# Optimization experiments

Measured on AMD Instinct MI355X. Metric: run time of the kernel, lower is better.

Reference implementation:

```python
import jax, jax.numpy as jnp
import numpy as np

BS, T, HS, WS = 2, 4, 32, 32
HW = HS * WS
D, NH, NL, NP = 256, 8, 4, 4
HD = D // NH
DFFN = 1024


def layer_norm(x, g, b, eps=1e-5):
    mu = jnp.mean(x, axis=-1, keepdims=True)
    var = jnp.mean((x - mu) ** 2, axis=-1, keepdims=True)
    return (x - mu) * jax.lax.rsqrt(var + eps) * g + b


def bilinear_gather(val, loc, Hl, Wl):
    # val: (bs, nh, Hl*Wl, hd); loc: (bs, Lq, nh, P, 2) in [0,1], last dim (x, y)
    # matches F.grid_sample(align_corners=False, padding_mode='zeros') on grid=2*loc-1
    x = loc[..., 0] * Wl - 0.5
    y = loc[..., 1] * Hl - 0.5
    x0 = jnp.floor(x)
    y0 = jnp.floor(y)
    lx = x - x0
    ly = y - y0
    bs, Lq, nh, P = x.shape
    out = jnp.zeros((bs, nh, Lq * P, val.shape[-1]), val.dtype)
    for dy in (0, 1):
        for dx in (0, 1):
            xi = x0 + dx
            yi = y0 + dy
            w = (lx if dx else 1.0 - lx) * (ly if dy else 1.0 - ly)
            valid = (xi >= 0) & (xi < Wl) & (yi >= 0) & (yi < Hl)
            w = jnp.where(valid, w, 0.0)
            xi_c = jnp.clip(xi, 0, Wl - 1).astype(jnp.int32)
            yi_c = jnp.clip(yi, 0, Hl - 1).astype(jnp.int32)
            idx = (yi_c * Wl + xi_c).transpose(0, 2, 1, 3).reshape(bs, nh, Lq * P)
            g = jnp.take_along_axis(val, idx[..., None], axis=2)
            wt = w.transpose(0, 2, 1, 3).reshape(bs, nh, Lq * P)
            out = out + wt[..., None] * g
    return out.reshape(bs, nh, Lq, P, val.shape[-1])


def setup_inputs() -> dict:
    key = jax.random.key(0)
    ks = jax.random.split(key, 12)
    s = 0.02
    return {
        "src": jax.random.normal(ks[0], (BS, T, HW, D), jnp.float32),
        "pos": jax.random.normal(ks[1], (BS, T, HW, D), jnp.float32),
        "reference_points": jax.random.uniform(ks[2], (BS, T * HW, NL, 2), jnp.float32),
        "value_proj_w": jax.random.normal(ks[3], (D, D), jnp.float32) * s,
        "value_proj_b": jnp.zeros((D,), jnp.float32),
        "sampling_offsets_w": jax.random.normal(ks[4], (D, NH * NL * NP * 2), jnp.float32) * s,
        "sampling_offsets_b": jax.random.normal(ks[5], (NH * NL * NP * 2,), jnp.float32) * s,
        "attn_weights_w": jax.random.normal(ks[6], (D, NH * NL * NP), jnp.float32) * s,
        "attn_weights_b": jnp.zeros((NH * NL * NP,), jnp.float32),
        "output_proj_w": jax.random.normal(ks[7], (D, D), jnp.float32) * s,
        "output_proj_b": jnp.zeros((D,), jnp.float32),
        "norm1_g": jnp.ones((D,), jnp.float32),
        "norm1_b": jnp.zeros((D,), jnp.float32),
        "linear1_w": jax.random.normal(ks[8], (D, DFFN), jnp.float32) * s,
        "linear1_b": jnp.zeros((DFFN,), jnp.float32),
        "linear2_w": jax.random.normal(ks[9], (DFFN, D), jnp.float32) * s,
        "linear2_b": jnp.zeros((D,), jnp.float32),
        "norm2_g": jnp.ones((D,), jnp.float32),
        "norm2_b": jnp.zeros((D,), jnp.float32),
        "spatial_shapes": np.array([[HS, WS]] * NL, np.int32),
        "level_start_index": np.arange(NL, dtype=np.int32) * HW,
    }


def reference(src, pos, reference_points, value_proj_w, value_proj_b,
              sampling_offsets_w, sampling_offsets_b, attn_weights_w, attn_weights_b,
              output_proj_w, output_proj_b, norm1_g, norm1_b,
              linear1_w, linear1_b, linear2_w, linear2_b, norm2_g, norm2_b,
              spatial_shapes, level_start_index):
    bs, t, hw, d = src.shape
    Lq = t * hw
    x = src.reshape(bs, Lq, d)
    q = x  # module never adds pos in forward (with_pos_embed unused)
    value = (x @ value_proj_w + value_proj_b).reshape(bs, Lq, NH, HD)
    offsets = (q @ sampling_offsets_w + sampling_offsets_b).reshape(bs, Lq, NH, NL, NP, 2)
    aw = jax.nn.softmax((q @ attn_weights_w + attn_weights_b).reshape(bs, Lq, NH, NL * NP), axis=-1)
    aw = aw.reshape(bs, Lq, NH, NL, NP)
    ss = np.asarray(spatial_shapes)
    lsi = np.asarray(level_start_index)
    offset_normalizer = jnp.asarray(ss[:, ::-1].copy(), src.dtype)  # (L, 2) = (W, H)
    sampling_locations = reference_points[:, :, None, :, None, :] + offsets / offset_normalizer[None, None, None, :, None, :]
    attn_out = jnp.zeros((bs, NH, Lq, HD), src.dtype)
    for l in range(NL):
        Hl, Wl = int(ss[l, 0]), int(ss[l, 1])
        start = int(lsi[l])
        v_l = value[:, start:start + Hl * Wl].transpose(0, 2, 1, 3)  # (bs, nh, HlWl, hd)
        samp = bilinear_gather(v_l, sampling_locations[:, :, :, l], Hl, Wl)  # (bs, nh, Lq, P, hd)
        w_l = aw[:, :, :, l].transpose(0, 2, 1, 3)  # (bs, nh, Lq, P)
        attn_out = attn_out + jnp.sum(samp * w_l[..., None], axis=3)
    attn_out = attn_out.transpose(0, 2, 1, 3).reshape(bs, Lq, d) @ output_proj_w + output_proj_b
    x = layer_norm(x + attn_out, norm1_g, norm1_b)
    ffn = jax.nn.relu(x @ linear1_w + linear1_b) @ linear2_w + linear2_b
    x = layer_norm(x + ffn, norm2_g, norm2_b)
    return x.reshape(bs, t, hw, d), sampling_locations
```

## Files before the change

### kernel.cpp

```cpp
#include <hip/hip_runtime.h>
#include <math.h>

#define ROWS   8192
#define LQ     4096
#define NHEAD  8
#define NLVL   4
#define NPTS   4
#define HDIM   32

typedef __attribute__((ext_vector_type(8))) short v8s;
typedef __attribute__((ext_vector_type(4))) float v4f;

__device__ __forceinline__ unsigned short f2bf(float x) {
    unsigned int u = __float_as_uint(x);
    u += 0x7fffu + ((u >> 16) & 1u);
    return (unsigned short)(u >> 16);
}
__device__ __forceinline__ float bf2f(unsigned short x) {
    return __uint_as_float(((unsigned int)x) << 16);
}

__device__ __forceinline__ void glds16(const void* g, void* l) {
    __builtin_amdgcn_global_load_lds(
        (const __attribute__((address_space(1))) unsigned int*)g,
        (__attribute__((address_space(3))) unsigned int*)l, 16, 0, 0);
}

__device__ __forceinline__ void trans_tile(const float* __restrict__ in,
                                           unsigned short* __restrict__ out,
                                           int K, int N, int ldout, int n_off,
                                           int bx, int by, int tid)
{
    __shared__ float t[32][33];
    int tx = tid & 31, ty = tid >> 5;
    int k0 = by << 5, n0 = bx << 5;
    #pragma unroll
    for (int i = 0; i < 4; i++)
        t[ty + i * 8][tx] = in[(size_t)(k0 + ty + i * 8) * N + n0 + tx];
    __syncthreads();
    #pragma unroll
    for (int i = 0; i < 4; i++)
        out[(size_t)(n_off + n0 + ty + i * 8) * ldout + k0 + tx] = f2bf(t[tx][ty + i * 8]);
}

__global__ __launch_bounds__(256) void prep_k(
    const float* __restrict__ src, unsigned short* __restrict__ src_bf,
    const float* __restrict__ vw, const float* __restrict__ ofw,
    const float* __restrict__ aww, const float* __restrict__ pw,
    const float* __restrict__ w1, const float* __restrict__ w2,
    unsigned short* __restrict__ Btcat, unsigned short* __restrict__ pwT,
    unsigned short* __restrict__ w1T, unsigned short* __restrict__ w2T,
    const float* __restrict__ vb, const float* __restrict__ ofb,
    const float* __restrict__ awb, float* __restrict__ biascat)
{
    int bid = blockIdx.x, tid = threadIdx.x;
    if (bid < 2048) {
        int i = bid * 256 + tid;
        float4 v = ((const float4*)src)[i];
        ushort4 o;
        o.x = f2bf(v.x); o.y = f2bf(v.y); o.z = f2bf(v.z); o.w = f2bf(v.w);
        ((ushort4*)src_bf)[i] = o;
    } else if (bid < 2112) {
        int t = bid - 2048; trans_tile(vw, Btcat, 256, 256, 256, 0, t & 7, t >> 3, tid);
    } else if (bid < 2176) {
        int t = bid - 2112; trans_tile(ofw, Btcat, 256, 256, 256, 256, t & 7, t >> 3, tid);
    } else if (bid < 2208) {
        int t = bid - 2176; trans_tile(aww, Btcat, 256, 128, 256, 512, t & 3, t >> 2, tid);
    } else if (bid < 2272) {
        int t = bid - 2208; trans_tile(pw, pwT, 256, 256, 256, 0, t & 7, t >> 3, tid);
    } else if (bid < 2528) {
        int t = bid - 2272; trans_tile(w1, w1T, 256, 1024, 256, 0, t & 31, t >> 5, tid);
    } else if (bid < 2784) {
        int t = bid - 2528; trans_tile(w2, w2T, 1024, 256, 1024, 0, t & 7, t >> 3, tid);
    } else {
        biascat[tid] = vb[tid];
        biascat[tid + 256] = ofb[tid];
        if (tid < 128) biascat[tid + 512] = awb[tid];
    }
}

template<bool PROJ, bool OUTBF, bool RELU, bool RES>
__global__ __launch_bounds__(256) void mfma_gemm_k(
    const unsigned short* __restrict__ A,
    const unsigned short* __restrict__ Bt,
    const float* __restrict__ bias,
    const float* __restrict__ res,
    void* __restrict__ Cout,
    unsigned short* __restrict__ vbf,
    int M, int N, int K)
{
    __shared__ __align__(16) unsigned short As[4096];
    __shared__ __align__(16) unsigned short Bs[2048];
    const int tid = threadIdx.x;
    const int row0 = blockIdx.y << 7, col0 = blockIdx.x << 6;
    const int wid = tid >> 6, lane = tid & 63;
    const int wm = wid & 1, wn = wid >> 1;
    const int lr = lane & 15, kq = lane >> 4;

    v4f acc[4][2];
    #pragma unroll
    for (int i = 0; i < 4; i++)
        #pragma unroll
        for (int j = 0; j < 2; j++) acc[i][j] = (v4f){0.f, 0.f, 0.f, 0.f};

    for (int k0 = 0; k0 < K; k0 += 32) {
        __syncthreads();
        #pragma unroll
        for (int i = 0; i < 2; i++) {
            int c = wid * 128 + i * 64 + lane;
            int row = c >> 2;
            int kk = ((c & 3) + (row >> 2)) & 3;
            glds16(A + (size_t)(row0 + row) * K + k0 + kk * 8,
                   &As[(wid * 128 + i * 64) * 8]);
        }
        {
            int c = wid * 64 + lane;
            int row = c >> 2;
            int kk = ((c & 3) + (row >> 2)) & 3;
            glds16(Bt + (size_t)(col0 + row) * K + k0 + kk * 8,
                   &Bs[wid * 512]);
        }
        __syncthreads();
        v8s bf[2];
        #pragma unroll
        for (int nt = 0; nt < 2; nt++) {
            int row = wn * 32 + nt * 16 + lr;
            int s = (kq - (row >> 2)) & 3;
            bf[nt] = *(const v8s*)(&Bs[(row * 4 + s) * 8]);
        }
        #pragma unroll
        for (int mt = 0; mt < 4; mt++) {
            int row = wm * 64 + mt * 16 + lr;
            int s = (kq - (row >> 2)) & 3;
            v8s af = *(const v8s*)(&As[(row * 4 + s) * 8]);
            #pragma unroll
            for (int nt = 0; nt < 2; nt++)
                acc[mt][nt] = __builtin_amdgcn_mfma_f32_16x16x32_bf16(af, bf[nt], acc[mt][nt], 0, 0, 0);
        }
    }

    const int rq = lane >> 4;
    #pragma unroll
    for (int mt = 0; mt < 4; mt++) {
        #pragma unroll
        for (int nt = 0; nt < 2; nt++) {
            int col = col0 + wn * 32 + nt * 16 + lr;
            float bv = bias[col];
            #pragma unroll
            for (int i = 0; i < 4; i++) {
                int row = row0 + wm * 64 + mt * 16 + rq * 4 + i;
                float v = acc[mt][nt][i] + bv;
                if (RELU) v = fmaxf(v, 0.f);
                if (RES)  v += res[(size_t)row * N + col];
                if (PROJ) {
                    if (col0 < 256) {
                        int b = row >> 12, rb = row & 4095;
                        int l = rb >> 10, pix = rb & 1023;
                        int h = col >> 5, d = col & 31;
                        size_t idx = ((size_t)(((b << 2) + l) * 8 + h) << 15) + (pix << 5) + d;
                        vbf[idx] = f2bf(v);
                    } else {
                        ((float*)Cout)[(size_t)row * 384 + col - 256] = v;
                    }
                } else if (OUTBF) {
                    ((unsigned short*)Cout)[(size_t)row * N + col] = f2bf(v);
                } else {
                    ((float*)Cout)[(size_t)row * N + col] = v;
                }
            }
        }
    }
}

__global__ __launch_bounds__(256) void fused_gather_k(
    const float* __restrict__ po,
    const unsigned short* __restrict__ vbf,
    const float* __restrict__ refp,
    float* __restrict__ out_loc,
    unsigned short* __restrict__ attn_bf)
{
    int tid = threadIdx.x;
    int u = tid >> 5, l = (tid >> 3) & 3, d4 = tid & 7;
    int h = blockIdx.x & 7;
    int r = (blockIdx.x >> 3) * 8 + u;
    int b = r >> 12;
    const float* prow = po + (size_t)r * 384;

    float2 rp = *(const float2*)(refp + (size_t)r * 8 + l * 2);

    float off[8];
    *(float4*)(off)     = *(const float4*)(prow + h * 32 + l * 8);
    *(float4*)(off + 4) = *(const float4*)(prow + h * 32 + l * 8 + 4);
    float locv[8];
    #pragma unroll
    for (int k = 0; k < 8; k++)
        locv[k] = ((k & 1) ? rp.y : rp.x) + off[k] * (1.f / 32.f);
    out_loc[(size_t)r * 256 + h * 32 + l * 8 + d4] = locv[d4];

    float w4[4];
    *(float4*)(w4) = *(const float4*)(prow + 256 + h * 16 + l * 4);
    float m = fmaxf(fmaxf(w4[0], w4[1]), fmaxf(w4[2], w4[3]));
    m = fmaxf(m, __shfl_xor(m, 8));
    m = fmaxf(m, __shfl_xor(m, 16));
    float s = 0.f;
    #pragma unroll
    for (int p = 0; p < 4; p++) { w4[p] = __expf(w4[p] - m); s += w4[p]; }
    s += __shfl_xor(s, 8);
    s += __shfl_xor(s, 16);
    float inv = 1.f / s;

    const unsigned short* vbase =
        vbf + (((size_t)(((b << 2) + l) * 8 + h)) << 15) + d4 * 4;
    ushort4 uv[16];
    float cw[16];
    #pragma unroll
    for (int p = 0; p < 4; p++) {
        float xf = locv[p * 2] * 32.f - 0.5f, yf = locv[p * 2 + 1] * 32.f - 0.5f;
        float x0f = floorf(xf), y0f = floorf(yf);
        float fx = xf - x0f, fy = yf - y0f;
        int x0 = (int)x0f, y0 = (int)y0f;
        float wgt = w4[p] * inv;
        #pragma unroll
        for (int dy = 0; dy < 2; dy++) {
            #pragma unroll
            for (int dx = 0; dx < 2; dx++) {
                int idx = p * 4 + dy * 2 + dx;
                int xi = x0 + dx, yi = y0 + dy;
                float wt = (dx ? fx : 1.f - fx) * (dy ? fy : 1.f - fy);
                bool valid = (xi >= 0) & (xi < 32) & (yi >= 0) & (yi < 32);
                int xc = min(max(xi, 0), 31), yc = min(max(yi, 0), 31);
                cw[idx] = valid ? (wgt * wt) : 0.f;
                uv[idx] = *(const ushort4*)(vbase + (size_t)((yc << 5) + xc) * 32);
            }
        }
    }
    float4 acc = {0.f, 0.f, 0.f, 0.f};
    #pragma unroll
    for (int idx = 0; idx < 16; idx++) {
        float c = cw[idx];
        acc.x += c * bf2f(uv[idx].x); acc.y += c * bf2f(uv[idx].y);
        acc.z += c * bf2f(uv[idx].z); acc.w += c * bf2f(uv[idx].w);
    }
    acc.x += __shfl_xor(acc.x, 8);  acc.y += __shfl_xor(acc.y, 8);
    acc.z += __shfl_xor(acc.z, 8);  acc.w += __shfl_xor(acc.w, 8);
    acc.x += __shfl_xor(acc.x, 16); acc.y += __shfl_xor(acc.y, 16);
    acc.z += __shfl_xor(acc.z, 16); acc.w += __shfl_xor(acc.w, 16);
    if (l == 0) {
        ushort4 o;
        o.x = f2bf(acc.x); o.y = f2bf(acc.y); o.z = f2bf(acc.z); o.w = f2bf(acc.w);
        *(ushort4*)(attn_bf + (size_t)r * 256 + h * 32 + d4 * 4) = o;
    }
}

template<bool WRITE_BF>
__global__ __launch_bounds__(256) void layernorm_k(
    float* __restrict__ x, const float* __restrict__ g, const float* __restrict__ b,
    unsigned short* __restrict__ xbf)
{
    int lane = threadIdx.x & 63;
    int wv = threadIdx.x >> 6;
    int row = blockIdx.x * 4 + wv;
    int c = lane << 2;
    float4 v = *(const float4*)(x + (size_t)row * 256 + c);
    float s = v.x + v.y + v.z + v.w;
    #pragma unroll
    for (int o = 1; o < 64; o <<= 1) s += __shfl_xor(s, o);
    float mu = s * (1.f / 256.f);
    float d0 = v.x - mu, d1 = v.y - mu, d2 = v.z - mu, d3 = v.w - mu;
    float vs = d0 * d0 + d1 * d1 + d2 * d2 + d3 * d3;
    #pragma unroll
    for (int o = 1; o < 64; o <<= 1) vs += __shfl_xor(vs, o);
    float rstd = rsqrtf(vs * (1.f / 256.f) + 1e-5f);
    float4 gg = *(const float4*)(g + c);
    float4 bb = *(const float4*)(b + c);
    float4 o4;
    o4.x = d0 * rstd * gg.x + bb.x;
    o4.y = d1 * rstd * gg.y + bb.y;
    o4.z = d2 * rstd * gg.z + bb.z;
    o4.w = d3 * rstd * gg.w + bb.w;
    *(float4*)(x + (size_t)row * 256 + c) = o4;
    if (WRITE_BF) {
        ushort4 ob;
        ob.x = f2bf(o4.x); ob.y = f2bf(o4.y); ob.z = f2bf(o4.z); ob.w = f2bf(o4.w);
        *(ushort4*)(xbf + (size_t)row * 256 + c) = ob;
    }
}

extern "C" void kernel_launch(void* const* d_in, const int* in_sizes, int n_in,
                              void* d_out, int out_size, void* d_ws, size_t ws_size,
                              hipStream_t stream)
{
    const float* src   = (const float*)d_in[0];
    const float* refp  = (const float*)d_in[2];
    const float* vw    = (const float*)d_in[3];
    const float* vb    = (const float*)d_in[4];
    const float* ofw   = (const float*)d_in[5];
    const float* ofb   = (const float*)d_in[6];
    const float* aww   = (const float*)d_in[7];
    const float* awb   = (const float*)d_in[8];
    const float* pw    = (const float*)d_in[9];
    const float* pb    = (const float*)d_in[10];
    const float* g1    = (const float*)d_in[11];
    const float* b1    = (const float*)d_in[12];
    const float* w1    = (const float*)d_in[13];
    const float* bi1   = (const float*)d_in[14];
    const float* w2    = (const float*)d_in[15];
    const float* bi2   = (const float*)d_in[16];
    const float* g2    = (const float*)d_in[17];
    const float* b2    = (const float*)d_in[18];

    float* ws = (float*)d_ws;
    float*          po        = ws;
    float*          x1        = ws + 3145728;
    unsigned short* value_bf  = (unsigned short*)(ws + 5242880);
    unsigned short* src_bf    = (unsigned short*)(ws + 6291456);
    unsigned short* x1_bf     = (unsigned short*)(ws + 7340032);
    unsigned short* attn_bf   = (unsigned short*)(ws + 8388608);
    unsigned short* hidden_bf = (unsigned short*)(ws + 9437184);
    unsigned short* Btcat     = (unsigned short*)(ws + 13631488);
    unsigned short* pwT       = (unsigned short*)(ws + 13713408);
    unsigned short* w1T       = (unsigned short*)(ws + 13746176);
    unsigned short* w2T       = (unsigned short*)(ws + 13877248);
    float*          biascat   = ws + 14008320;

    float* out_x   = (float*)d_out;
    float* out_loc = out_x + 2097152;

    dim3 blk(256);

    prep_k<<<2785, blk, 0, stream>>>(src, src_bf, vw, ofw, aww, pw, w1, w2,
                                     Btcat, pwT, w1T, w2T, vb, ofb, awb, biascat);

    mfma_gemm_k<true, false, false, false><<<dim3(10, 64), blk, 0, stream>>>(
        src_bf, Btcat, biascat, nullptr, po, value_bf, ROWS, 640, 256);

    fused_gather_k<<<8192, blk, 0, stream>>>(po, value_bf, refp, out_loc, attn_bf);

    mfma_gemm_k<false, false, false, true><<<dim3(4, 64), blk, 0, stream>>>(
        attn_bf, pwT, pb, src, x1, nullptr, ROWS, 256, 256);
    layernorm_k<true><<<2048, blk, 0, stream>>>(x1, g1, b1, x1_bf);

    mfma_gemm_k<false, true, true, false><<<dim3(16, 64), blk, 0, stream>>>(
        x1_bf, w1T, bi1, nullptr, hidden_bf, nullptr, ROWS, 1024, 256);
    mfma_gemm_k<false, false, false, true><<<dim3(4, 64), blk, 0, stream>>>(
        hidden_bf, w2T, bi2, x1, out_x, nullptr, ROWS, 256, 1024);
    layernorm_k<false><<<2048, blk, 0, stream>>>(out_x, g2, b2, nullptr);
}
```

Baseline: 189.3 us.

## Fuse sampling-location compute into projection GEMM epilogue; add 64-row GEMM for N=256

```diff
diff --git a/kernel.cpp b/kernel.cpp
--- a/kernel.cpp
+++ b/kernel.cpp
@@ -87,6 +87,8 @@
     const float* __restrict__ res,
     void* __restrict__ Cout,
     unsigned short* __restrict__ vbf,
+    const float* __restrict__ refp,
+    float* __restrict__ oloc,
     int M, int N, int K)
 {
     __shared__ __align__(16) unsigned short As[4096];
@@ -159,8 +161,13 @@
                         int h = col >> 5, d = col & 31;
                         size_t idx = ((size_t)(((b << 2) + l) * 8 + h) << 15) + (pix << 5) + d;
                         vbf[idx] = f2bf(v);
+                    } else if (col0 < 512) {
+                        int colm = col - 256;
+                        int l = (colm >> 3) & 3, cc = colm & 1;
+                        oloc[(size_t)row * 256 + colm] =
+                            refp[(size_t)row * 8 + l * 2 + cc] + v * (1.f / 32.f);
                     } else {
-                        ((float*)Cout)[(size_t)row * 384 + col - 256] = v;
+                        ((float*)Cout)[(size_t)row * 128 + col - 512] = v;
                     }
                 } else if (OUTBF) {
                     ((unsigned short*)Cout)[(size_t)row * N + col] = f2bf(v);
@@ -172,11 +179,69 @@
     }
 }
 
+template<bool OUTBF, bool RELU, bool RES>
+__global__ __launch_bounds__(256) void mfma_gemm64_k(
+    const unsigned short* __restrict__ A,
+    const unsigned short* __restrict__ Bt,
+    const float* __restrict__ bias,
+    const float* __restrict__ res,
+    void* __restrict__ Cout,
+    int M, int N, int K)
+{
+    __shared__ __align__(16) unsigned short As[2048];
+    __shared__ __align__(16) unsigned short Bs[2048];
+    const int tid = threadIdx.x;
+    const int row0 = blockIdx.y << 6, col0 = blockIdx.x << 6;
+    const int wid = tid >> 6, lane = tid & 63;
+    const int lr = lane & 15, kq = lane >> 4;
+
+    v4f acc[4];
+    #pragma unroll
+    for (int i = 0; i < 4; i++) acc[i] = (v4f){0.f, 0.f, 0.f, 0.f};
+
+    for (int k0 = 0; k0 < K; k0 += 32) {
+        __syncthreads();
+        {
+            int c = wid * 64 + lane;
+            int row = c >> 2;
+            int kk = ((c & 3) + (row >> 2)) & 3;
+            glds16(A + (size_t)(row0 + row) * K + k0 + kk * 8, &As[wid * 512]);
+            glds16(Bt + (size_t)(col0 + row) * K + k0 + kk * 8, &Bs[wid * 512]);
+        }
+        __syncthreads();
+        int colr = wid * 16 + lr;
+        int sb = (kq - (colr >> 2)) & 3;
+        v8s bf = *(const v8s*)(&Bs[(colr * 4 + sb) * 8]);
+        #pragma unroll
+        for (int mt = 0; mt < 4; mt++) {
+            int rowr = mt * 16 + lr;
+            int sa = (kq - (rowr >> 2)) & 3;
+            v8s af = *(const v8s*)(&As[(rowr * 4 + sa) * 8]);
+            acc[mt] = __builtin_amdgcn_mfma_f32_16x16x32_bf16(af, bf, acc[mt], 0, 0, 0);
+        }
+    }
+
+    const int rq = lane >> 4;
+    const int col = col0 + wid * 16 + lr;
+    float bv = bias[col];
+    #pragma unroll
+    for (int mt = 0; mt < 4; mt++) {
+        #pragma unroll
+        for (int i = 0; i < 4; i++) {
+            int row = row0 + mt * 16 + rq * 4 + i;
+            float v = acc[mt][i] + bv;
+            if (RELU) v = fmaxf(v, 0.f);
+            if (RES)  v += res[(size_t)row * N + col];
+            if (OUTBF) ((unsigned short*)Cout)[(size_t)row * N + col] = f2bf(v);
+            else       ((float*)Cout)[(size_t)row * N + col] = v;
+        }
+    }
+}
+
 __global__ __launch_bounds__(256) void fused_gather_k(
     const float* __restrict__ po,
     const unsigned short* __restrict__ vbf,
-    const float* __restrict__ refp,
-    float* __restrict__ out_loc,
+    const float* __restrict__ loc,
     unsigned short* __restrict__ attn_bf)
 {
     int tid = threadIdx.x;
@@ -184,21 +249,13 @@
     int h = blockIdx.x & 7;
     int r = (blockIdx.x >> 3) * 8 + u;
     int b = r >> 12;
-    const float* prow = po + (size_t)r * 384;
-
-    float2 rp = *(const float2*)(refp + (size_t)r * 8 + l * 2);
-
-    float off[8];
-    *(float4*)(off)     = *(const float4*)(prow + h * 32 + l * 8);
-    *(float4*)(off + 4) = *(const float4*)(prow + h * 32 + l * 8 + 4);
+
     float locv[8];
-    #pragma unroll
-    for (int k = 0; k < 8; k++)
-        locv[k] = ((k & 1) ? rp.y : rp.x) + off[k] * (1.f / 32.f);
-    out_loc[(size_t)r * 256 + h * 32 + l * 8 + d4] = locv[d4];
+    *(float4*)(locv)     = *(const float4*)(loc + (size_t)r * 256 + h * 32 + l * 8);
+    *(float4*)(locv + 4) = *(const float4*)(loc + (size_t)r * 256 + h * 32 + l * 8 + 4);
 
     float w4[4];
-    *(float4*)(w4) = *(const float4*)(prow + 256 + h * 16 + l * 4);
+    *(float4*)(w4) = *(const float4*)(po + (size_t)r * 128 + h * 16 + l * 4);
     float m = fmaxf(fmaxf(w4[0], w4[1]), fmaxf(w4[2], w4[3]));
     m = fmaxf(m, __shfl_xor(m, 8));
     m = fmaxf(m, __shfl_xor(m, 16));
@@ -311,17 +368,17 @@
 
     float* ws = (float*)d_ws;
     float*          po        = ws;
-    float*          x1        = ws + 3145728;
-    unsigned short* value_bf  = (unsigned short*)(ws + 5242880);
-    unsigned short* src_bf    = (unsigned short*)(ws + 6291456);
-    unsigned short* x1_bf     = (unsigned short*)(ws + 7340032);
-    unsigned short* attn_bf   = (unsigned short*)(ws + 8388608);
-    unsigned short* hidden_bf = (unsigned short*)(ws + 9437184);
-    unsigned short* Btcat     = (unsigned short*)(ws + 13631488);
-    unsigned short* pwT       = (unsigned short*)(ws + 13713408);
-    unsigned short* w1T       = (unsigned short*)(ws + 13746176);
-    unsigned short* w2T       = (unsigned short*)(ws + 13877248);
-    float*          biascat   = ws + 14008320;
+    float*          x1        = ws + 1048576;
+    unsigned short* value_bf  = (unsigned short*)(ws + 3145728);
+    unsigned short* src_bf    = (unsigned short*)(ws + 4194304);
+    unsigned short* x1_bf     = (unsigned short*)(ws + 5242880);
+    unsigned short* attn_bf   = (unsigned short*)(ws + 6291456);
+    unsigned short* hidden_bf = (unsigned short*)(ws + 7340032);
+    unsigned short* Btcat     = (unsigned short*)(ws + 11534336);
+    unsigned short* pwT       = (unsigned short*)(ws + 11616256);
+    unsigned short* w1T       = (unsigned short*)(ws + 11649024);
+    unsigned short* w2T       = (unsigned short*)(ws + 11780096);
+    float*          biascat   = ws + 11911168;
 
     float* out_x   = (float*)d_out;
     float* out_loc = out_x + 2097152;
@@ -332,17 +389,17 @@
                                      Btcat, pwT, w1T, w2T, vb, ofb, awb, biascat);
 
     mfma_gemm_k<true, false, false, false><<<dim3(10, 64), blk, 0, stream>>>(
-        src_bf, Btcat, biascat, nullptr, po, value_bf, ROWS, 640, 256);
-
-    fused_gather_k<<<8192, blk, 0, stream>>>(po, value_bf, refp, out_loc, attn_bf);
-
-    mfma_gemm_k<false, false, false, true><<<dim3(4, 64), blk, 0, stream>>>(
-        attn_bf, pwT, pb, src, x1, nullptr, ROWS, 256, 256);
+        src_bf, Btcat, biascat, nullptr, po, value_bf, refp, out_loc, ROWS, 640, 256);
+
+    fused_gather_k<<<8192, blk, 0, stream>>>(po, value_bf, out_loc, attn_bf);
+
+    mfma_gemm64_k<false, false, true><<<dim3(4, 128), blk, 0, stream>>>(
+        attn_bf, pwT, pb, src, x1, ROWS, 256, 256);
     layernorm_k<true><<<2048, blk, 0, stream>>>(x1, g1, b1, x1_bf);
 
     mfma_gemm_k<false, true, true, false><<<dim3(16, 64), blk, 0, stream>>>(
-        x1_bf, w1T, bi1, nullptr, hidden_bf, nullptr, ROWS, 1024, 256);
-    mfma_gemm_k<false, false, false, true><<<dim3(4, 64), blk, 0, stream>>>(
-        hidden_bf, w2T, bi2, x1, out_x, nullptr, ROWS, 256, 1024);
+        x1_bf, w1T, bi1, nullptr, hidden_bf, nullptr, nullptr, nullptr, ROWS, 1024, 256);
+    mfma_gemm64_k<false, false, true><<<dim3(4, 128), blk, 0, stream>>>(
+        hidden_bf, w2T, bi2, x1, out_x, ROWS, 256, 1024);
     layernorm_k<false><<<2048, blk, 0, stream>>>(out_x, g2, b2, nullptr);
 }
```

Measured after the change: 189.2 us. No clear change (-0.0%).
